# Performance work log

Measured on AMD Instinct MI355X. Metric: run time of the kernel, lower is better.

## Reference

```python
import jax, jax.numpy as jnp
import numpy as np
from jax import lax

B, H, W_IN, C = 32, 32, 32, 128   # NHWC input
KH, KW = 3, 3                     # kernel size (padding 'same', stride 1)
F = 512                           # filters


def setup_inputs() -> dict:
    key = jax.random.key(0)
    ks = jax.random.split(key, 10)
    # sparse factor shapes: (KH*KW*C, 1152), (1152, F), (F, F)
    d0, d1, d2, d3 = KH * KW * C, 1152, F, F
    x = jax.random.normal(ks[0], (B, H, W_IN, C), dtype=jnp.float32)
    k0 = jax.random.normal(ks[1], (d0, d1), dtype=jnp.float32) * (1.0 / np.sqrt(d0))
    k1 = jax.random.normal(ks[2], (d1, d2), dtype=jnp.float32) * (1.0 / np.sqrt(d1))
    k2 = jax.random.normal(ks[3], (d2, d3), dtype=jnp.float32) * (1.0 / np.sqrt(d2))
    # fixed binary sparsity masks (K.constant in the original build)
    m0 = jax.random.bernoulli(ks[4], 0.1, (d0, d1)).astype(jnp.float32)
    m1 = jax.random.bernoulli(ks[5], 0.1, (d1, d2)).astype(jnp.float32)
    m2 = jax.random.bernoulli(ks[6], 0.1, (d2, d3)).astype(jnp.float32)
    scale = jax.random.normal(ks[7], (1,), dtype=jnp.float32)
    bias = jax.random.normal(ks[8], (F,), dtype=jnp.float32) * 0.01
    return {"x": x, "k0": k0, "k1": k1, "k2": k2,
            "m0": m0, "m1": m1, "m2": m2, "scale": scale, "bias": bias}


def reference(x, k0, k1, k2, m0, m1, m2, scale, bias):
    # Chained masked sparse factors collapse (associativity) to one effective
    # filter matrix of shape (KH*KW*C, F); the im2col row flatten order in the
    # original is (h, w, c), which matches an HWIO reshape exactly.
    w_eff = (k0 * m0) @ (k1 * m1) @ (k2 * m2)          # (KH*KW*C, F)
    w = (w_eff * scale[0]).reshape(KH, KW, C, F)        # fold scalar scale into kernel
    out = lax.conv_general_dilated(
        x, w, window_strides=(1, 1), padding='SAME',
        dimension_numbers=('NHWC', 'HWIO', 'NHWC'))     # (B, H, W, F)
    return out + bias
```

## Files before the change

kernel.cpp:

```cpp
#include <hip/hip_runtime.h>

typedef __attribute__((ext_vector_type(8))) short short8;
typedef __attribute__((ext_vector_type(4))) float f32x4;

typedef __attribute__((address_space(1))) const unsigned gas_u32;
typedef __attribute__((address_space(3))) unsigned las_u32;

static __device__ __forceinline__ void g2l16(const void* g, void* l) {
  __builtin_amdgcn_global_load_lds((gas_u32*)g, (las_u32*)l, 16, 0, 0);
}

static __device__ __forceinline__ short f2bf(float f) {
  union { float f; unsigned u; } v; v.f = f;
  unsigned r = (v.u + 0x7FFFu + ((v.u >> 16) & 1u)) >> 16;
  return (short)r;
}

#define MF(a_, b_, c_) __builtin_amdgcn_mfma_f32_16x16x32_bf16(a_, b_, c_, 0, 0, 0)

static __device__ __forceinline__ void xcvt_body(const float* __restrict__ x,
                                                 short* __restrict__ xbp, int i) {
  int c8 = i & 15;
  int t = i >> 4;
  int wp = t % 34, t2 = t / 34;
  int hp = t2 % 34, b = t2 / 34;
  short8 o = {};
  if (hp >= 1 && hp <= 32 && wp >= 1 && wp <= 32) {
    const f32x4* s = (const f32x4*)(x + (((size_t)((b << 5) + hp - 1) << 5) + (wp - 1)) * 128 + c8 * 8);
    f32x4 a = s[0], bb2 = s[1];
    o[0] = f2bf(a[0]); o[1] = f2bf(a[1]); o[2] = f2bf(a[2]); o[3] = f2bf(a[3]);
    o[4] = f2bf(bb2[0]); o[5] = f2bf(bb2[1]); o[6] = f2bf(bb2[2]); o[7] = f2bf(bb2[3]);
  }
  ((short8*)xbp)[i] = o;
}

__global__ __launch_bounds__(256) void k_prepw(const float* __restrict__ k0f,
                                               const float* __restrict__ m0f,
                                               const float* __restrict__ scf,
                                               const float* __restrict__ k1f,
                                               const float* __restrict__ m1f,
                                               const float* __restrict__ k2f,
                                               const float* __restrict__ m2f,
                                               short* __restrict__ w1b,
                                               short* __restrict__ w2T,
                                               short* __restrict__ w3T,
                                               const float* __restrict__ x,
                                               short* __restrict__ xbp) {
  __shared__ float tile[32][33];
  const int bb = blockIdx.x, tid = threadIdx.x;
  if (bb < 648) {
    int i = bb * 256 + tid;
    float s = scf[0];
    const f32x4* kk = (const f32x4*)k0f + (size_t)i * 2;
    const f32x4* mm = (const f32x4*)m0f + (size_t)i * 2;
    f32x4 a0 = kk[0], a1 = kk[1], b0 = mm[0], b1 = mm[1];
    short8 o;
    o[0] = f2bf(a0[0] * b0[0] * s); o[1] = f2bf(a0[1] * b0[1] * s);
    o[2] = f2bf(a0[2] * b0[2] * s); o[3] = f2bf(a0[3] * b0[3] * s);
    o[4] = f2bf(a1[0] * b1[0] * s); o[5] = f2bf(a1[1] * b1[1] * s);
    o[6] = f2bf(a1[2] * b1[2] * s); o[7] = f2bf(a1[3] * b1[3] * s);
    ((short8*)w1b)[i] = o;
  } else if (bb < 1480) {
    const float *kf, *mf; short* outp; int D, F, idx;
    if (bb < 1224) { kf = k1f; mf = m1f; outp = w2T; D = 1152; F = 512; idx = bb - 648; }
    else           { kf = k2f; mf = m2f; outp = w3T; D = 512;  F = 512; idx = bb - 1224; }
    int f0 = (idx & 15) * 32, d0 = (idx >> 4) * 32;
    int tx = tid & 31, ty = tid >> 5;
#pragma unroll
    for (int i = 0; i < 4; ++i) {
      int d = d0 + ty + i * 8;
      size_t ix = (size_t)d * F + f0 + tx;
      tile[ty + i * 8][tx] = kf[ix] * mf[ix];
    }
    __syncthreads();
#pragma unroll
    for (int i = 0; i < 4; ++i) {
      int f = f0 + ty + i * 8;
      outp[(size_t)f * D + d0 + tx] = f2bf(tile[tx][ty + i * 8]);
    }
  } else {
    xcvt_body(x, xbp, (bb - 1480) * 256 + tid);
  }
}

__global__ __launch_bounds__(256) void k_gemmx(const short* __restrict__ A,
                                               const short* __restrict__ BT,
                                               short* __restrict__ C, int M, int N, int K,
                                               const float* __restrict__ x,
                                               short* __restrict__ xbp, int xoff) {
  __shared__ __align__(16) short As[2][64][128];
  __shared__ __align__(16) short Bs[2][64][128];
  if (blockIdx.x >= 144) {
    xcvt_body(x, xbp, (xoff + (int)blockIdx.x - 144) * 256 + (int)threadIdx.x);
    return;
  }
  const int ntiles = N >> 6;
  const int m0 = (blockIdx.x / ntiles) << 6, n0 = (blockIdx.x % ntiles) << 6;
  const int tid = threadIdx.x;
  const int lane = tid & 63, wv = tid >> 6;
  const int wr = (wv >> 1) * 32, wc = (wv & 1) * 32;
  const int lr = lane & 15, lh = lane >> 4;

  const int rr = tid >> 4, sl = tid & 15;
  const int swz = sl ^ (rr & 7);
  const unsigned aOff = (unsigned)(m0 + rr) * K + swz * 8;
  const unsigned bOff = (unsigned)(n0 + rr) * K + swz * 8;
  const int ldsRow = 4 * wv;

  f32x4 acc[2][2] = {};

#define GST(buf_, kt_) do { \
    _Pragma("unroll") for (int j = 0; j < 4; ++j) \
      g2l16(A + aOff + (unsigned)j * 16u * (unsigned)K + (unsigned)(kt_) * 128u, \
            &As[buf_][j * 16 + ldsRow][0]); \
    _Pragma("unroll") for (int j = 0; j < 4; ++j) \
      g2l16(BT + bOff + (unsigned)j * 16u * (unsigned)K + (unsigned)(kt_) * 128u, \
            &Bs[buf_][j * 16 + ldsRow][0]); \
  } while (0)

  const int nk = K >> 7;
  GST(0, 0);
  asm volatile("s_waitcnt vmcnt(0)" ::: "memory");
  __builtin_amdgcn_s_barrier();

  for (int kt = 0; kt < nk; ++kt) {
    const int cur = kt & 1;
    if (kt + 1 < nk) { if (cur) GST(0, kt + 1); else GST(1, kt + 1); }
#pragma unroll
    for (int ks = 0; ks < 4; ++ks) {
      short8 af[2], bf[2];
#pragma unroll
      for (int i = 0; i < 2; ++i)
        af[i] = *(const short8*)&As[cur][wr + i * 16 + lr][((ks * 4 + lh) ^ (lr & 7)) * 8];
#pragma unroll
      for (int i = 0; i < 2; ++i)
        bf[i] = *(const short8*)&Bs[cur][wc + i * 16 + lr][((ks * 4 + lh) ^ (lr & 7)) * 8];
#pragma unroll
      for (int mi = 0; mi < 2; ++mi)
#pragma unroll
        for (int ni = 0; ni < 2; ++ni)
          acc[mi][ni] = MF(af[mi], bf[ni], acc[mi][ni]);
    }
    if (kt + 1 < nk) asm volatile("s_waitcnt vmcnt(0)" ::: "memory");
    __builtin_amdgcn_s_barrier();
  }
#pragma unroll
  for (int mi = 0; mi < 2; ++mi) {
    const int row = m0 + wr + mi * 16 + lh * 4;
#pragma unroll
    for (int ni = 0; ni < 2; ++ni) {
      const int col = n0 + wc + ni * 16 + lr;
#pragma unroll
      for (int q = 0; q < 4; ++q)
        C[(size_t)(row + q) * N + col] = f2bf(acc[mi][ni][q]);
    }
  }
#undef GST
}

#define RD_A(mf_, ks_) \
  (*(const short8*)&As[wr * 128 + (mf_) * 16 + lr][(((ks_) * 4 + lh) ^ (lr & 7)) * 8])
#define RD_B(nf_, ks_) \
  (*(const short8*)&Bs[wc * 32 + (nf_) * 16 + lr][(((ks_) * 4 + lh) ^ (lr & 7)) * 8])

#define LOADB do { \
  bfr[0][0] = RD_B(0, 0); bfr[0][1] = RD_B(0, 1); \
  bfr[1][0] = RD_B(1, 0); bfr[1][1] = RD_B(1, 1); } while (0)

#define STAGE_AQ(q_, tt_) do { \
  const int tc_ = (tt_) > 17 ? 17 : (tt_); \
  const int khw_ = tc_ >> 1; const int kh_ = (khw_ * 11) >> 5; const int kw_ = khw_ - kh_ * 3; \
  const int ao_ = (kh_ * 34 + kw_) * 128 + ((tc_ & 1) << 6) + (q_) * 4352; \
  g2l16(xbp + aBase + ao_, &As[aRow + (q_) * 32][0]); } while (0)

#define STAGE_BH(j_, tt_) do { \
  const int tc_ = (tt_) > 17 ? 17 : (tt_); \
  g2l16(wT + bBase + (j_) * 73728 + tc_ * 64, &Bs[(j_) * 64 + bRow][0]); } while (0)

#define MFMA8(p_) \
  acc[2*(p_)  ][0] = MF(a0k0, bfr[0][0], acc[2*(p_)  ][0]); \
  acc[2*(p_)  ][1] = MF(a0k0, bfr[1][0], acc[2*(p_)  ][1]); \
  acc[2*(p_)+1][0] = MF(a1k0, bfr[0][0], acc[2*(p_)+1][0]); \
  acc[2*(p_)+1][1] = MF(a1k0, bfr[1][0], acc[2*(p_)+1][1]); \
  acc[2*(p_)  ][0] = MF(a0k1, bfr[0][1], acc[2*(p_)  ][0]); \
  acc[2*(p_)  ][1] = MF(a0k1, bfr[1][1], acc[2*(p_)  ][1]); \
  acc[2*(p_)+1][0] = MF(a1k1, bfr[0][1], acc[2*(p_)+1][0]); \
  acc[2*(p_)+1][1] = MF(a1k1, bfr[1][1], acc[2*(p_)+1][1]);

#define VM2 asm volatile("s_waitcnt vmcnt(2)" ::: "memory")

#define PHASE(p_, PRE, ...) do { \
  PRE; \
  short8 a0k0 = RD_A(2*(p_), 0),   a0k1 = RD_A(2*(p_), 1); \
  short8 a1k0 = RD_A(2*(p_)+1, 0), a1k1 = RD_A(2*(p_)+1, 1); \
  __VA_ARGS__ \
  asm volatile("s_waitcnt lgkmcnt(0)" ::: "memory"); \
  __builtin_amdgcn_sched_barrier(0); \
  __builtin_amdgcn_s_setprio(1); \
  MFMA8(p_) \
  __builtin_amdgcn_s_setprio(0); \
  VM2; \
  __builtin_amdgcn_s_barrier(); \
} while (0)

__global__ __launch_bounds__(512, 4) void k_conv(const short* __restrict__ xbp,
                                                 const short* __restrict__ wT,
                                                 const float* __restrict__ bias,
                                                 float* __restrict__ out) {
  __shared__ __align__(16) short As[256][64];
  __shared__ __align__(16) short Bs[128][64];
  int bid = blockIdx.x;
  bid = (bid & 7) * 64 + (bid >> 3);
  const int mt = bid >> 2, nt = bid & 3;
  const int m0 = mt << 8, n0 = nt << 7;
  const int tid = threadIdx.x;
  const int lane = tid & 63, wid = tid >> 6;
  const int wr = wid >> 2, wc = wid & 3;
  const int lr = lane & 15, lh = lane >> 4;

  f32x4 acc[8][2] = {};
  short8 bfr[2][2];

  const int wrB = (wid >> 2) * 128;
  const int rsub = (wid & 3) * 8 + (lane >> 3);
  const int sw = (lane & 7) ^ (lane >> 3);
  const int aRow = wrB + (wid & 3) * 8;
  const int bRow = wid * 8;

  const int Mb = m0 + wrB + rsub;
  const int b = Mb >> 10, h0 = (Mb >> 5) & 31, w = Mb & 31;
  const unsigned aBase = (unsigned)((b * 34 + h0) * 34 + w) * 128 + sw * 8;
  const unsigned bBase = (unsigned)(n0 + wid * 8 + (lane >> 3)) * 1152 + sw * 8;

  STAGE_BH(0, 0); STAGE_BH(1, 0);
  STAGE_AQ(0, 0); STAGE_AQ(1, 0); STAGE_AQ(2, 0);
  asm volatile("s_waitcnt vmcnt(0)" ::: "memory");
  __builtin_amdgcn_s_barrier();

  for (int t = 0; t < 18; ++t) {
    const int tn = t + 1;
    PHASE(0, LOADB, STAGE_AQ(3, t););
    PHASE(1, ,      STAGE_BH(0, tn); STAGE_BH(1, tn););
    PHASE(2, ,      STAGE_AQ(0, tn); STAGE_AQ(1, tn););
    PHASE(3, ,      STAGE_AQ(2, tn););
  }
  asm volatile("s_waitcnt vmcnt(0)" ::: "memory");

  const int orow = m0 + wr * 128, ocol = n0 + wc * 32;
#pragma unroll
  for (int mf = 0; mf < 8; ++mf) {
    const int row = orow + mf * 16 + lh * 4;
#pragma unroll
    for (int nf = 0; nf < 2; ++nf) {
      const int col = ocol + nf * 16 + lr;
      const float bv = bias[col];
#pragma unroll
      for (int q = 0; q < 4; ++q)
        out[(size_t)(row + q) * 512 + col] = acc[mf][nf][q] + bv;
    }
  }
}

extern "C" void kernel_launch(void* const* d_in, const int* in_sizes, int n_in,
                              void* d_out, int out_size, void* d_ws, size_t ws_size,
                              hipStream_t stream) {
  (void)in_sizes; (void)n_in; (void)out_size; (void)ws_size;
  const float* x    = (const float*)d_in[0];
  const float* k0   = (const float*)d_in[1];
  const float* k1   = (const float*)d_in[2];
  const float* k2   = (const float*)d_in[3];
  const float* m0   = (const float*)d_in[4];
  const float* m1   = (const float*)d_in[5];
  const float* m2   = (const float*)d_in[6];
  const float* sc   = (const float*)d_in[7];
  const float* bias = (const float*)d_in[8];
  float* out = (float*)d_out;
  char* ws = (char*)d_ws;

  short* xbp = (short*)(ws);
  short* w1b = (short*)(ws + 9469952);
  short* w2T = (short*)(ws + 12124160);
  short* w3T = (short*)(ws + 13303808);
  short* A1b = (short*)(ws + 13828096);
  short* wET = (short*)(ws + 15007744);

  k_prepw<<<2248, 256, 0, stream>>>(k0, m0, sc, k1, m1, k2, m2, w1b, w2T, w3T, x, xbp);
  k_gemmx<<<916, 256, 0, stream>>>(w1b, w2T, A1b, 1152, 512, 1152, x, xbp, 768);
  k_gemmx<<<916, 256, 0, stream>>>(w3T, A1b, wET, 512, 1152, 512, x, xbp, 1540);
  k_conv<<<512, 512, 0, stream>>>(xbp, wET, bias, out);
}
```

Before: 69.74 us.

## Halve conv block to 4 waves with 128x64 per-wave tiles

The conv kernel drops from 8 waves to 4 waves per block, keeping the same 256x128 block tile. Each wave now computes 128x64 outputs instead of 128x32, which doubles the B fragments held in registers and the MFMAs issued per LDS A read. Each thread issues twice as many async global-to-LDS loads, and the vmcnt waits are retuned to match. This raises register use and lowers the number of waves available to hide latency, in exchange for more reuse of each LDS fragment and fewer barrier participants.

New measurement: 69.28 us. Within noise of the previous version (-0.6%).

```diff
diff --git a/kernel.cpp b/kernel.cpp
--- a/kernel.cpp
+++ b/kernel.cpp
@@ -161,35 +161,47 @@
 #define RD_A(mf_, ks_) \
   (*(const short8*)&As[wr * 128 + (mf_) * 16 + lr][(((ks_) * 4 + lh) ^ (lr & 7)) * 8])
 #define RD_B(nf_, ks_) \
-  (*(const short8*)&Bs[wc * 32 + (nf_) * 16 + lr][(((ks_) * 4 + lh) ^ (lr & 7)) * 8])
+  (*(const short8*)&Bs[wc * 64 + (nf_) * 16 + lr][(((ks_) * 4 + lh) ^ (lr & 7)) * 8])
 
 #define LOADB do { \
   bfr[0][0] = RD_B(0, 0); bfr[0][1] = RD_B(0, 1); \
-  bfr[1][0] = RD_B(1, 0); bfr[1][1] = RD_B(1, 1); } while (0)
+  bfr[1][0] = RD_B(1, 0); bfr[1][1] = RD_B(1, 1); \
+  bfr[2][0] = RD_B(2, 0); bfr[2][1] = RD_B(2, 1); \
+  bfr[3][0] = RD_B(3, 0); bfr[3][1] = RD_B(3, 1); } while (0)
 
 #define STAGE_AQ(q_, tt_) do { \
   const int tc_ = (tt_) > 17 ? 17 : (tt_); \
   const int khw_ = tc_ >> 1; const int kh_ = (khw_ * 11) >> 5; const int kw_ = khw_ - kh_ * 3; \
   const int ao_ = (kh_ * 34 + kw_) * 128 + ((tc_ & 1) << 6) + (q_) * 4352; \
-  g2l16(xbp + aBase + ao_, &As[aRow + (q_) * 32][0]); } while (0)
-
-#define STAGE_BH(j_, tt_) do { \
+  g2l16(xbp + aBase + ao_, &As[(q_) * 32 + ldsA][0]); \
+  g2l16(xbp + aBase + 17408 + ao_, &As[128 + (q_) * 32 + ldsA][0]); } while (0)
+
+#define STAGE_B(tt_) do { \
   const int tc_ = (tt_) > 17 ? 17 : (tt_); \
-  g2l16(wT + bBase + (j_) * 73728 + tc_ * 64, &Bs[(j_) * 64 + bRow][0]); } while (0)
-
-#define MFMA8(p_) \
+  g2l16(wT + bBase +     tc_ * 64, &Bs[     ldsA][0]); \
+  g2l16(wT + bBase + 36864 + tc_ * 64, &Bs[32 + ldsA][0]); \
+  g2l16(wT + bBase + 73728 + tc_ * 64, &Bs[64 + ldsA][0]); \
+  g2l16(wT + bBase + 110592 + tc_ * 64, &Bs[96 + ldsA][0]); } while (0)
+
+#define MFMA16(p_) \
   acc[2*(p_)  ][0] = MF(a0k0, bfr[0][0], acc[2*(p_)  ][0]); \
   acc[2*(p_)  ][1] = MF(a0k0, bfr[1][0], acc[2*(p_)  ][1]); \
+  acc[2*(p_)  ][2] = MF(a0k0, bfr[2][0], acc[2*(p_)  ][2]); \
+  acc[2*(p_)  ][3] = MF(a0k0, bfr[3][0], acc[2*(p_)  ][3]); \
   acc[2*(p_)+1][0] = MF(a1k0, bfr[0][0], acc[2*(p_)+1][0]); \
   acc[2*(p_)+1][1] = MF(a1k0, bfr[1][0], acc[2*(p_)+1][1]); \
+  acc[2*(p_)+1][2] = MF(a1k0, bfr[2][0], acc[2*(p_)+1][2]); \
+  acc[2*(p_)+1][3] = MF(a1k0, bfr[3][0], acc[2*(p_)+1][3]); \
   acc[2*(p_)  ][0] = MF(a0k1, bfr[0][1], acc[2*(p_)  ][0]); \
   acc[2*(p_)  ][1] = MF(a0k1, bfr[1][1], acc[2*(p_)  ][1]); \
+  acc[2*(p_)  ][2] = MF(a0k1, bfr[2][1], acc[2*(p_)  ][2]); \
+  acc[2*(p_)  ][3] = MF(a0k1, bfr[3][1], acc[2*(p_)  ][3]); \
   acc[2*(p_)+1][0] = MF(a1k1, bfr[0][1], acc[2*(p_)+1][0]); \
-  acc[2*(p_)+1][1] = MF(a1k1, bfr[1][1], acc[2*(p_)+1][1]);
-
-#define VM2 asm volatile("s_waitcnt vmcnt(2)" ::: "memory")
-
-#define PHASE(p_, PRE, ...) do { \
+  acc[2*(p_)+1][1] = MF(a1k1, bfr[1][1], acc[2*(p_)+1][1]); \
+  acc[2*(p_)+1][2] = MF(a1k1, bfr[2][1], acc[2*(p_)+1][2]); \
+  acc[2*(p_)+1][3] = MF(a1k1, bfr[3][1], acc[2*(p_)+1][3]);
+
+#define PHASE(p_, PRE, WAITV, ...) do { \
   PRE; \
   short8 a0k0 = RD_A(2*(p_), 0),   a0k1 = RD_A(2*(p_), 1); \
   short8 a1k0 = RD_A(2*(p_)+1, 0), a1k1 = RD_A(2*(p_)+1, 1); \
@@ -197,13 +209,17 @@
   asm volatile("s_waitcnt lgkmcnt(0)" ::: "memory"); \
   __builtin_amdgcn_sched_barrier(0); \
   __builtin_amdgcn_s_setprio(1); \
-  MFMA8(p_) \
+  MFMA16(p_) \
   __builtin_amdgcn_s_setprio(0); \
-  VM2; \
+  WAITV; \
   __builtin_amdgcn_s_barrier(); \
 } while (0)
 
-__global__ __launch_bounds__(512, 4) void k_conv(const short* __restrict__ xbp,
+#define VM4 asm volatile("s_waitcnt vmcnt(4)" ::: "memory")
+#define VM6 asm volatile("s_waitcnt vmcnt(6)" ::: "memory")
+#define VM8 asm volatile("s_waitcnt vmcnt(8)" ::: "memory")
+
+__global__ __launch_bounds__(256, 2) void k_conv(const short* __restrict__ xbp,
                                                  const short* __restrict__ wT,
                                                  const float* __restrict__ bias,
                                                  float* __restrict__ out) {
@@ -215,43 +231,41 @@
   const int m0 = mt << 8, n0 = nt << 7;
   const int tid = threadIdx.x;
   const int lane = tid & 63, wid = tid >> 6;
-  const int wr = wid >> 2, wc = wid & 3;
+  const int wr = wid >> 1, wc = wid & 1;
   const int lr = lane & 15, lh = lane >> 4;
 
-  f32x4 acc[8][2] = {};
-  short8 bfr[2][2];
-
-  const int wrB = (wid >> 2) * 128;
-  const int rsub = (wid & 3) * 8 + (lane >> 3);
-  const int sw = (lane & 7) ^ (lane >> 3);
-  const int aRow = wrB + (wid & 3) * 8;
-  const int bRow = wid * 8;
-
-  const int Mb = m0 + wrB + rsub;
+  f32x4 acc[8][4] = {};
+  short8 bfr[4][2];
+
+  const int rsub = tid >> 3;
+  const int sw = (tid & 7) ^ (rsub & 7);
+  const int ldsA = wid * 8;
+
+  const int Mb = m0 + rsub;
   const int b = Mb >> 10, h0 = (Mb >> 5) & 31, w = Mb & 31;
   const unsigned aBase = (unsigned)((b * 34 + h0) * 34 + w) * 128 + sw * 8;
-  const unsigned bBase = (unsigned)(n0 + wid * 8 + (lane >> 3)) * 1152 + sw * 8;
-
-  STAGE_BH(0, 0); STAGE_BH(1, 0);
+  const unsigned bBase = (unsigned)(n0 + rsub) * 1152 + sw * 8;
+
+  STAGE_B(0);
   STAGE_AQ(0, 0); STAGE_AQ(1, 0); STAGE_AQ(2, 0);
   asm volatile("s_waitcnt vmcnt(0)" ::: "memory");
   __builtin_amdgcn_s_barrier();
 
   for (int t = 0; t < 18; ++t) {
     const int tn = t + 1;
-    PHASE(0, LOADB, STAGE_AQ(3, t););
-    PHASE(1, ,      STAGE_BH(0, tn); STAGE_BH(1, tn););
-    PHASE(2, ,      STAGE_AQ(0, tn); STAGE_AQ(1, tn););
-    PHASE(3, ,      STAGE_AQ(2, tn););
+    PHASE(0, LOADB, VM4, STAGE_AQ(3, t););
+    PHASE(1, ,      VM6, STAGE_B(tn););
+    PHASE(2, ,      VM8, STAGE_AQ(0, tn); STAGE_AQ(1, tn););
+    PHASE(3, ,      VM4, STAGE_AQ(2, tn););
   }
   asm volatile("s_waitcnt vmcnt(0)" ::: "memory");
 
-  const int orow = m0 + wr * 128, ocol = n0 + wc * 32;
+  const int orow = m0 + wr * 128, ocol = n0 + wc * 64;
 #pragma unroll
   for (int mf = 0; mf < 8; ++mf) {
     const int row = orow + mf * 16 + lh * 4;
 #pragma unroll
-    for (int nf = 0; nf < 2; ++nf) {
+    for (int nf = 0; nf < 4; ++nf) {
       const int col = ocol + nf * 16 + lr;
       const float bv = bias[col];
 #pragma unroll
@@ -287,5 +301,5 @@
   k_prepw<<<2248, 256, 0, stream>>>(k0, m0, sc, k1, m1, k2, m2, w1b, w2T, w3T, x, xbp);
   k_gemmx<<<916, 256, 0, stream>>>(w1b, w2T, A1b, 1152, 512, 1152, x, xbp, 768);
   k_gemmx<<<916, 256, 0, stream>>>(w3T, A1b, wET, 512, 1152, 512, x, xbp, 1540);
-  k_conv<<<512, 512, 0, stream>>>(xbp, wET, bias, out);
-}
+  k_conv<<<512, 256, 0, stream>>>(xbp, wET, bias, out);
+}
```
